# Optimization experiments

Measured on AMD Instinct MI355X. Metric: run time of the kernel, lower is better.

The kernel has to match this reference:

```python
import jax, jax.numpy as jnp
import numpy as np

K_NEIGHBOURS = 2


def setup_inputs() -> dict:
    key = jax.random.key(0)
    k1, k2 = jax.random.split(key)
    train_features = jax.random.normal(k1, (200000, 128), dtype=jnp.float32)
    test_features = jax.random.normal(k2, (2048, 128), dtype=jnp.float32)
    return {"train_features": train_features, "test_features": test_features}


def reference(train_features, test_features):
    # faiss IndexFlatL2 returns SQUARED L2 distances.
    # d2[m, n] = ||q_m||^2 + ||t_n||^2 - 2 q_m . t_n
    q_sq = jnp.sum(test_features * test_features, axis=1, keepdims=True)   # [M, 1]
    t_sq = jnp.sum(train_features * train_features, axis=1)                # [N]
    cross = jnp.einsum('md,nd->mn', test_features, train_features)        # [M, N]
    d2 = q_sq + t_sq[None, :] - 2.0 * cross                               # [M, N]
    # top-2 smallest distances per query -> negate and take top_k
    neg_topk, _ = jax.lax.top_k(-d2, K_NEIGHBOURS)                        # [M, 2]
    # sum of the 2 nearest-neighbour squared distances
    return jnp.sum(-neg_topk, axis=1)                                     # [M]
```

## Files before the change

### kernel.cpp

```cpp
#include <hip/hip_runtime.h>
#include <hip/hip_bf16.h>


typedef short bf16x8 __attribute__((ext_vector_type(8)));
typedef float f32x4 __attribute__((ext_vector_type(4)));

#define N_TRAIN 200000
#define M_QUERY 2048
#define DIMS 128

__device__ __forceinline__ unsigned int bf_bits(float f) {
  unsigned int u = __float_as_uint(f);
  return (u + 0x7FFFu + ((u >> 16) & 1u)) >> 16;
}

__global__ __launch_bounds__(256) void convert_kernel(
    const float* __restrict__ src, unsigned short* __restrict__ dst,
    float* __restrict__ sq, int nrows, float scale) {
  int gtid = blockIdx.x * 256 + threadIdx.x;
  int row = gtid >> 3, sub = gtid & 7;
  if (row >= nrows) return;
  const float4* s4 = reinterpret_cast<const float4*>(src + (size_t)row * DIMS + sub * 16);
  unsigned int pk[8];
  float acc = 0.f;
#pragma unroll
  for (int i = 0; i < 4; ++i) {
    float4 v = s4[i];
    acc += v.x * v.x + v.y * v.y + v.z * v.z + v.w * v.w;
    pk[i * 2 + 0] = bf_bits(v.x * scale) | (bf_bits(v.y * scale) << 16);
    pk[i * 2 + 1] = bf_bits(v.z * scale) | (bf_bits(v.w * scale) << 16);
  }
  uint4* d4 = reinterpret_cast<uint4*>(dst + (size_t)row * DIMS + sub * 16);
  d4[0] = make_uint4(pk[0], pk[1], pk[2], pk[3]);
  d4[1] = make_uint4(pk[4], pk[5], pk[6], pk[7]);
  acc += __shfl_xor(acc, 1);
  acc += __shfl_xor(acc, 2);
  acc += __shfl_xor(acc, 4);
  if (sub == 0) sq[row] = acc;
}

template <int NCH>
__global__ __launch_bounds__(64) void knn_main(
    const unsigned short* __restrict__ tb, const unsigned short* __restrict__ qb16,
    const float* __restrict__ tsq, float* __restrict__ partials) {
  constexpr int PPC = N_TRAIN / NCH;
  constexpr int ITERS = PPC / 16;
  const int b = blockIdx.x;
  const int g = (b & 7) * (NCH * 4) + (b >> 3);
  const int chunk = g >> 5;
  const int qw = (g & 31) << 6;
  const int l = threadIdx.x;
  const int lo = l & 15, hi = l >> 4;

  __shared__ char smem[2 * 4096];

  bf16x8 a[4][4];
#pragma unroll
  for (int t = 0; t < 4; ++t)
#pragma unroll
    for (int kf = 0; kf < 4; ++kf)
      a[t][kf] = *reinterpret_cast<const bf16x8*>(
          qb16 + (size_t)(qw + t * 16 + lo) * DIMS + kf * 32 + hi * 8);

  const int offE = hi * 256 + ((lo ^ hi) << 4);
  const int offO = (4 + hi) * 256 + ((lo ^ (4 + hi)) << 4);
  const char* gt = reinterpret_cast<const char*>(tb) + (size_t)chunk * PPC * 256;
  const float* tq = tsq + chunk * PPC;

  int roff[4];
#pragma unroll
  for (int kf = 0; kf < 4; ++kf)
    roff[kf] = lo * 256 + ((((kf << 2) + hi) ^ (lo & 7)) << 4);

  const float INF = __builtin_inff();
  float best1[4][4], best2[4][4];
#pragma unroll
  for (int t = 0; t < 4; ++t)
#pragma unroll
    for (int r = 0; r < 4; ++r) { best1[t][r] = INF; best2[t][r] = INF; }

#define ISSUE(T, P, TV)                                                        \
  do {                                                                         \
    const char* _s = gt + (size_t)(T) * 4096;                                  \
    char* _d = smem + (P) * 4096;                                              \
    __builtin_amdgcn_global_load_lds(                                          \
        (const __attribute__((address_space(1))) void*)(_s + offE),            \
        (__attribute__((address_space(3))) void*)_d, 16, 0, 0);                \
    __builtin_amdgcn_global_load_lds(                                          \
        (const __attribute__((address_space(1))) void*)(_s + offO),            \
        (__attribute__((address_space(3))) void*)(_d + 1024), 16, 0, 0);       \
    __builtin_amdgcn_global_load_lds(                                          \
        (const __attribute__((address_space(1))) void*)(_s + 2048 + offE),     \
        (__attribute__((address_space(3))) void*)(_d + 2048), 16, 0, 0);       \
    __builtin_amdgcn_global_load_lds(                                          \
        (const __attribute__((address_space(1))) void*)(_s + 2048 + offO),     \
        (__attribute__((address_space(3))) void*)(_d + 3072), 16, 0, 0);       \
    TV = tq[(T) * 16 + lo];                                                    \
  } while (0)

#define COMPUTE(P, TV)                                                         \
  do {                                                                         \
    const char* _buf = smem + (P) * 4096;                                      \
    bf16x8 f[4];                                                               \
    _Pragma("unroll")                                                          \
    for (int kf = 0; kf < 4; ++kf)                                             \
      f[kf] = *reinterpret_cast<const bf16x8*>(_buf + roff[kf]);               \
    f32x4 c = {TV, TV, TV, TV};                                                \
    _Pragma("unroll")                                                          \
    for (int t = 0; t < 4; ++t) {                                              \
      f32x4 acc = __builtin_amdgcn_mfma_f32_16x16x32_bf16(a[t][0], f[0], c, 0, 0, 0); \
      acc = __builtin_amdgcn_mfma_f32_16x16x32_bf16(a[t][1], f[1], acc, 0, 0, 0);     \
      acc = __builtin_amdgcn_mfma_f32_16x16x32_bf16(a[t][2], f[2], acc, 0, 0, 0);     \
      acc = __builtin_amdgcn_mfma_f32_16x16x32_bf16(a[t][3], f[3], acc, 0, 0, 0);     \
      _Pragma("unroll")                                                        \
      for (int r = 0; r < 4; ++r) {                                            \
        float s0 = acc[r];             \
        float n1 = fminf(best1[t][r], s0);                                     \
        float n2 = __builtin_amdgcn_fmed3f(best1[t][r], best2[t][r], s0);      \
        best1[t][r] = n1;                                                      \
        best2[t][r] = n2;                                                      \
      }                                                                        \
    }                                                                          \
  } while (0)

  float tvA, tvB;
  ISSUE(0, 0, tvA);
  ISSUE(1, 1, tvB);

  for (int it = 0; it + 2 < ITERS; it += 2) {
    asm volatile("s_waitcnt vmcnt(5)" ::: "memory");
    COMPUTE(0, tvA);
    ISSUE(it + 2, 0, tvA);
    asm volatile("s_waitcnt vmcnt(5)" ::: "memory");
    COMPUTE(1, tvB);
    ISSUE(it + 3, 1, tvB);
  }
  asm volatile("s_waitcnt vmcnt(5)" ::: "memory");
  COMPUTE(0, tvA);
  asm volatile("s_waitcnt vmcnt(0)" ::: "memory");
  COMPUTE(1, tvB);

#undef ISSUE
#undef COMPUTE

#pragma unroll
  for (int t = 0; t < 4; ++t)
#pragma unroll
    for (int r = 0; r < 4; ++r) {
      float v1 = best1[t][r], v2 = best2[t][r];
#pragma unroll
      for (int m = 1; m < 16; m <<= 1) {
        float o1 = __shfl_xor(v1, m);
        float o2 = __shfl_xor(v2, m);
        float n1 = fminf(v1, o1);
        float n2 = fminf(fmaxf(v1, o1), fminf(v2, o2));
        v1 = n1;
        v2 = n2;
      }
      best1[t][r] = v1;
      best2[t][r] = v2;
    }
  if (lo == 0) {
#pragma unroll
    for (int t = 0; t < 4; ++t)
#pragma unroll
      for (int r = 0; r < 4; ++r) {
        int q = qw + t * 16 + hi * 4 + r;
        float* p = partials + ((size_t)chunk * M_QUERY + q) * 2;
        p[0] = best1[t][r];
        p[1] = best2[t][r];
      }
  }
}

__global__ __launch_bounds__(256) void knn_reduce(
    const float* __restrict__ partials, const float* __restrict__ qsq,
    float* __restrict__ out, int nchunk) {
  int q = blockIdx.x * 256 + threadIdx.x;
  if (q >= M_QUERY) return;
  const float INF = __builtin_inff();
  float b1 = INF, b2 = INF;
  for (int c = 0; c < nchunk; ++c) {
    const float* p = partials + ((size_t)c * M_QUERY + q) * 2;
    float v = p[0];
    float n1 = fminf(b1, v);
    float n2 = __builtin_amdgcn_fmed3f(b1, b2, v);
    b1 = n1; b2 = n2;
    v = p[1];
    n1 = fminf(b1, v);
    n2 = __builtin_amdgcn_fmed3f(b1, b2, v);
    b1 = n1; b2 = n2;
  }
  out[q] = 2.f * qsq[q] + b1 + b2;
}

extern "C" void kernel_launch(void* const* d_in, const int* in_sizes, int n_in,
                              void* d_out, int out_size, void* d_ws, size_t ws_size,
                              hipStream_t stream) {
  const float* train = (const float*)d_in[0];
  const float* test  = (const float*)d_in[1];
  float* out = (float*)d_out;
  char* ws = (char*)d_ws;

  size_t off_tb  = 0;
  size_t off_qb  = off_tb  + (size_t)N_TRAIN * DIMS * 2;
  size_t off_tsq = off_qb  + (size_t)M_QUERY * DIMS * 2;
  size_t off_qsq = off_tsq + (size_t)N_TRAIN * 4;
  size_t off_pt  = off_qsq + (size_t)M_QUERY * 4;
  size_t need125 = off_pt + (size_t)125 * M_QUERY * 2 * 4;
  if (ws_size < need125) return;

  unsigned short* tbp = (unsigned short*)(ws + off_tb);
  unsigned short* qb  = (unsigned short*)(ws + off_qb);
  float* tsq = (float*)(ws + off_tsq);
  float* qsq = (float*)(ws + off_qsq);
  float* part = (float*)(ws + off_pt);

  hipLaunchKernelGGL(convert_kernel, dim3((N_TRAIN * 8) / 256), dim3(256), 0, stream,
                     train, tbp, tsq, N_TRAIN, 1.0f);
  hipLaunchKernelGGL(convert_kernel, dim3((M_QUERY * 8) / 256), dim3(256), 0, stream,
                     test, qb, qsq, M_QUERY, -2.0f);
  hipLaunchKernelGGL(knn_main<125>, dim3(125 * 32), dim3(64), 0, stream,
                     tbp, qb, tsq, part);
  hipLaunchKernelGGL(knn_reduce, dim3(M_QUERY / 256), dim3(256), 0, stream,
                     part, qsq, out, 125);
}
```

Baseline: 202.7 us.

## Use 4-wave blocks with register double-buffered LDS reads and MFMA priority

Merges four independent 64-thread workgroups into one 256-thread block. Each wave keeps its own LDS double buffer and handles 64 queries of a shared 256-query block. The main loop is restructured to prefetch the next tile's fragments from LDS into registers while the MFMAs for the current tile run. s_setprio is raised around the MFMA/top-2 section. The aim is to overlap LDS read latency with matrix math and improve scheduling, at the cost of more registers for the second fragment set and explicit lgkmcnt waits.

```diff
diff --git a/kernel.cpp b/kernel.cpp
--- a/kernel.cpp
+++ b/kernel.cpp
@@ -8,6 +8,9 @@
 #define N_TRAIN 200000
 #define M_QUERY 2048
 #define DIMS 128
+#define NCH 125
+#define PPC (N_TRAIN / NCH)
+#define ITERS (PPC / 16)
 
 __device__ __forceinline__ unsigned int bf_bits(float f) {
   unsigned int u = __float_as_uint(f);
@@ -39,20 +42,20 @@
   if (sub == 0) sq[row] = acc;
 }
 
-template <int NCH>
-__global__ __launch_bounds__(64) void knn_main(
+__global__ __launch_bounds__(256) void knn_main(
     const unsigned short* __restrict__ tb, const unsigned short* __restrict__ qb16,
     const float* __restrict__ tsq, float* __restrict__ partials) {
-  constexpr int PPC = N_TRAIN / NCH;
-  constexpr int ITERS = PPC / 16;
   const int b = blockIdx.x;
-  const int g = (b & 7) * (NCH * 4) + (b >> 3);
-  const int chunk = g >> 5;
-  const int qw = (g & 31) << 6;
-  const int l = threadIdx.x;
+  const int g = (b & 7) * NCH + (b >> 3);
+  const int chunk = g >> 3;
+  const int qblock = (g & 7) << 8;
+  const int tid = threadIdx.x;
+  const int w = tid >> 6, l = tid & 63;
   const int lo = l & 15, hi = l >> 4;
-
-  __shared__ char smem[2 * 4096];
+  const int qw = qblock + w * 64;
+
+  __shared__ char smem[4][2 * 4096];
+  char* lbase = smem[w];
 
   bf16x8 a[4][4];
 #pragma unroll
@@ -79,10 +82,10 @@
 #pragma unroll
     for (int r = 0; r < 4; ++r) { best1[t][r] = INF; best2[t][r] = INF; }
 
-#define ISSUE(T, P, TV)                                                        \
+#define ISSUE(T, BUF, TV)                                                      \
   do {                                                                         \
     const char* _s = gt + (size_t)(T) * 4096;                                  \
-    char* _d = smem + (P) * 4096;                                              \
+    char* _d = lbase + (BUF) * 4096;                                           \
     __builtin_amdgcn_global_load_lds(                                          \
         (const __attribute__((address_space(1))) void*)(_s + offE),            \
         (__attribute__((address_space(3))) void*)_d, 16, 0, 0);                \
@@ -98,20 +101,25 @@
     TV = tq[(T) * 16 + lo];                                                    \
   } while (0)
 
-#define COMPUTE(P, TV)                                                         \
+#define READF(F, BUF)                                                          \
   do {                                                                         \
-    const char* _buf = smem + (P) * 4096;                                      \
-    bf16x8 f[4];                                                               \
-    _Pragma("unroll")                                                          \
-    for (int kf = 0; kf < 4; ++kf)                                             \
-      f[kf] = *reinterpret_cast<const bf16x8*>(_buf + roff[kf]);               \
+    const char* _buf = lbase + (BUF) * 4096;                                   \
+    F[0] = *reinterpret_cast<const bf16x8*>(_buf + roff[0]);                   \
+    F[1] = *reinterpret_cast<const bf16x8*>(_buf + roff[1]);                   \
+    F[2] = *reinterpret_cast<const bf16x8*>(_buf + roff[2]);                   \
+    F[3] = *reinterpret_cast<const bf16x8*>(_buf + roff[3]);                   \
+  } while (0)
+
+#define MFMA_TOP2(F, TV)                                                       \
+  do {                                                                         \
     f32x4 c = {TV, TV, TV, TV};                                                \
+    __builtin_amdgcn_s_setprio(1);                                             \
     _Pragma("unroll")                                                          \
     for (int t = 0; t < 4; ++t) {                                              \
-      f32x4 acc = __builtin_amdgcn_mfma_f32_16x16x32_bf16(a[t][0], f[0], c, 0, 0, 0); \
-      acc = __builtin_amdgcn_mfma_f32_16x16x32_bf16(a[t][1], f[1], acc, 0, 0, 0);     \
-      acc = __builtin_amdgcn_mfma_f32_16x16x32_bf16(a[t][2], f[2], acc, 0, 0, 0);     \
-      acc = __builtin_amdgcn_mfma_f32_16x16x32_bf16(a[t][3], f[3], acc, 0, 0, 0);     \
+      f32x4 acc = __builtin_amdgcn_mfma_f32_16x16x32_bf16(a[t][0], F[0], c, 0, 0, 0); \
+      acc = __builtin_amdgcn_mfma_f32_16x16x32_bf16(a[t][1], F[1], acc, 0, 0, 0);     \
+      acc = __builtin_amdgcn_mfma_f32_16x16x32_bf16(a[t][2], F[2], acc, 0, 0, 0);     \
+      acc = __builtin_amdgcn_mfma_f32_16x16x32_bf16(a[t][3], F[3], acc, 0, 0, 0);     \
       _Pragma("unroll")                                                        \
       for (int r = 0; r < 4; ++r) {                                            \
         float s0 = acc[r];             \
@@ -121,27 +129,45 @@
         best2[t][r] = n2;                                                      \
       }                                                                        \
     }                                                                          \
+    __builtin_amdgcn_s_setprio(0);                                             \
   } while (0)
 
+  bf16x8 fA[4], fB[4];
   float tvA, tvB;
   ISSUE(0, 0, tvA);
   ISSUE(1, 1, tvB);
-
-  for (int it = 0; it + 2 < ITERS; it += 2) {
-    asm volatile("s_waitcnt vmcnt(5)" ::: "memory");
-    COMPUTE(0, tvA);
-    ISSUE(it + 2, 0, tvA);
-    asm volatile("s_waitcnt vmcnt(5)" ::: "memory");
-    COMPUTE(1, tvB);
-    ISSUE(it + 3, 1, tvB);
-  }
   asm volatile("s_waitcnt vmcnt(5)" ::: "memory");
-  COMPUTE(0, tvA);
-  asm volatile("s_waitcnt vmcnt(0)" ::: "memory");
-  COMPUTE(1, tvB);
+  READF(fA, 0);
+
+  for (int it = 0; it + 3 < ITERS; it += 2) {
+    {
+      float t0 = tvA;
+      asm volatile("s_waitcnt lgkmcnt(0)" ::: "memory");
+      ISSUE(it + 2, 0, tvA);
+      asm volatile("s_waitcnt vmcnt(5)" ::: "memory");
+      READF(fB, 1);
+      MFMA_TOP2(fA, t0);
+    }
+    {
+      float t1 = tvB;
+      asm volatile("s_waitcnt lgkmcnt(0)" ::: "memory");
+      ISSUE(it + 3, 1, tvB);
+      asm volatile("s_waitcnt vmcnt(5)" ::: "memory");
+      READF(fA, 0);
+      MFMA_TOP2(fB, t1);
+    }
+  }
+  {
+    float t0 = tvA;
+    asm volatile("s_waitcnt vmcnt(0)" ::: "memory");
+    READF(fB, 1);
+    MFMA_TOP2(fA, t0);
+    MFMA_TOP2(fB, tvB);
+  }
 
 #undef ISSUE
-#undef COMPUTE
+#undef READF
+#undef MFMA_TOP2
 
 #pragma unroll
   for (int t = 0; t < 4; ++t)
@@ -207,7 +233,7 @@
   size_t off_tsq = off_qb  + (size_t)M_QUERY * DIMS * 2;
   size_t off_qsq = off_tsq + (size_t)N_TRAIN * 4;
   size_t off_pt  = off_qsq + (size_t)M_QUERY * 4;
-  size_t need125 = off_pt + (size_t)125 * M_QUERY * 2 * 4;
+  size_t need125 = off_pt + (size_t)NCH * M_QUERY * 2 * 4;
   if (ws_size < need125) return;
 
   unsigned short* tbp = (unsigned short*)(ws + off_tb);
@@ -220,8 +246,8 @@
                      train, tbp, tsq, N_TRAIN, 1.0f);
   hipLaunchKernelGGL(convert_kernel, dim3((M_QUERY * 8) / 256), dim3(256), 0, stream,
                      test, qb, qsq, M_QUERY, -2.0f);
-  hipLaunchKernelGGL(knn_main<125>, dim3(125 * 32), dim3(64), 0, stream,
+  hipLaunchKernelGGL(knn_main, dim3(NCH * 8), dim3(256), 0, stream,
                      tbp, qb, tsq, part);
   hipLaunchKernelGGL(knn_reduce, dim3(M_QUERY / 256), dim3(256), 0, stream,
-                     part, qsq, out, 125);
-}
+                     part, qsq, out, NCH);
+}
```

After: 203.0 us. About the same (+0.2%).
